# Kernel tuning notes

Hardware: AMD Instinct MI355X
Metric: run time of the kernel (lower is better)

## Reference

```python
import jax, jax.numpy as jnp
import numpy as np

EMBED = 1024
HEADS = 16
HEAD_DIM = EMBED // HEADS


def setup_inputs() -> dict:
    key = jax.random.key(0)
    ks = jax.random.split(key, 5)
    s = 0.02
    x = jax.random.normal(ks[0], (2, 2048, EMBED), dtype=jnp.float32)
    W_qkv = jax.random.normal(ks[1], (EMBED, 3 * EMBED), dtype=jnp.float32) * s
    b_qkv = jnp.zeros((3 * EMBED,), dtype=jnp.float32)
    W_proj = jax.random.normal(ks[2], (EMBED, EMBED), dtype=jnp.float32) * s
    b_proj = jnp.zeros((EMBED,), dtype=jnp.float32)
    return {"x": x, "W_qkv": W_qkv, "b_qkv": b_qkv, "W_proj": W_proj, "b_proj": b_proj}


def reference(x, W_qkv, b_qkv, W_proj, b_proj):
    B, N, _ = x.shape
    scale = HEAD_DIM ** -0.5
    qkv = x @ W_qkv + b_qkv                     # [B,N,3E]
    qkv = qkv.reshape(B, N, 3, HEADS, HEAD_DIM)
    q = qkv[:, :, 0].transpose(0, 2, 1, 3) * scale  # [B,H,N,D]
    k = qkv[:, :, 1].transpose(0, 2, 1, 3)
    v = qkv[:, :, 2].transpose(0, 2, 1, 3)
    attn = jnp.einsum('bhnd,bhmd->bhnm', q, k)  # [B,H,N,N]
    attn = jax.nn.softmax(attn, axis=-1)
    out = jnp.einsum('bhnm,bhmd->bhnd', attn, v)  # [B,H,N,D]
    out = out.transpose(0, 2, 1, 3).reshape(B, N, HEADS * HEAD_DIM)
    return out @ W_proj + b_proj
```

## Files before the change

### kernel.cpp

```cpp
#include <hip/hip_runtime.h>
#include <hip/hip_bf16.h>
#include <stdint.h>

typedef unsigned short u16;
typedef __bf16 bf16x8 __attribute__((ext_vector_type(8)));
typedef float f32x4 __attribute__((ext_vector_type(4)));

__device__ __forceinline__ u16 f2bf(float f) {
    union { float f; unsigned u; } x; x.f = f;
    unsigned u = x.u;
    u += 0x7FFFu + ((u >> 16) & 1u);
    return (u16)(u >> 16);
}

typedef __attribute__((address_space(1))) void gvoid;
typedef __attribute__((address_space(3))) void lvoid;
__device__ __forceinline__ void gl2lds16(const void* g, void* l) {
    __builtin_amdgcn_global_load_lds((gvoid*)g, (lvoid*)l, 16, 0, 0);
}

__global__ __launch_bounds__(256) void prep_kernel(
    const float* __restrict__ x, u16* __restrict__ xb,
    const float* __restrict__ Wqkv, u16* __restrict__ wqkvT,
    const float* __restrict__ Wproj, u16* __restrict__ wprojT)
{
    __shared__ u16 tile[64][65];
    const int blk = blockIdx.x;
    const int tid = threadIdx.x;

    if (blk < 2048) {
        const size_t i = ((size_t)blk * 256 + tid) * 8;
        float4 a = *(const float4*)(x + i);
        float4 b = *(const float4*)(x + i + 4);
        ushort4 oa, ob;
        oa.x = f2bf(a.x); oa.y = f2bf(a.y); oa.z = f2bf(a.z); oa.w = f2bf(a.w);
        ob.x = f2bf(b.x); ob.y = f2bf(b.y); ob.z = f2bf(b.z); ob.w = f2bf(b.w);
        *(ushort4*)(xb + i) = oa;
        *(ushort4*)(xb + i + 4) = ob;
        return;
    }
    const float* in; u16* out; int rows, cols, bx, by;
    if (blk < 2816) { int t = blk - 2048; in = Wqkv;  out = wqkvT;  rows = 1024; cols = 3072; bx = t % 48; by = t / 48; }
    else            { int t = blk - 2816; in = Wproj; out = wprojT; rows = 1024; cols = 1024; bx = t % 16; by = t / 16; }
#pragma unroll
    for (int i = 0; i < 16; i++) {
        int e = i * 256 + tid;
        int r = e >> 6, c = e & 63;
        tile[r][c] = f2bf(in[(size_t)(by * 64 + r) * cols + bx * 64 + c]);
    }
    __syncthreads();
#pragma unroll
    for (int i = 0; i < 16; i++) {
        int e = i * 256 + tid;
        int r = e >> 6, c = e & 63;
        out[(size_t)(bx * 64 + r) * rows + by * 64 + c] = tile[c][r];
    }
}

__global__ __launch_bounds__(256) void transpose_v(
    const u16* __restrict__ in, u16* __restrict__ out)
{
    __shared__ u16 tile[64][65];
    const int bh = blockIdx.y;
    const int t0 = blockIdx.x * 64;
    const u16* ip = in + ((size_t)bh * 2048 + t0) * 64;
    u16* op = out + (size_t)bh * 64 * 2048 + t0;
    const int tid = threadIdx.x;
#pragma unroll
    for (int i = 0; i < 16; i++) {
        int e = i * 256 + tid;
        int r = e >> 6, c = e & 63;
        tile[r][c] = ip[(size_t)r * 64 + c];
    }
    __syncthreads();
#pragma unroll
    for (int i = 0; i < 16; i++) {
        int e = i * 256 + tid;
        int d = e >> 6, tt = e & 63;
        op[(size_t)d * 2048 + tt] = tile[tt][d];
    }
}

__global__ __launch_bounds__(256) void gemm_qkv(
    const u16* __restrict__ A, const u16* __restrict__ Bt,
    const float* __restrict__ bias,
    u16* __restrict__ q, u16* __restrict__ ko, u16* __restrict__ vo)
{
    constexpr int K = 1024;
    __shared__ __align__(16) u16 smem[128 * 132];
    u16* sA = smem;
    u16* sB = smem + 8192;
    const int tid = threadIdx.x;
    const int wave = tid >> 6, lane = tid & 63;
    const int quad = lane >> 4, l16 = lane & 15;
    const int wm = (wave >> 1) * 64, wn = (wave & 1) * 64;
    const int m0 = blockIdx.y * 128, n0 = blockIdx.x * 128;
    const int srow = lane >> 3;
    const int scol = (lane & 7) * 8;

    f32x4 acc[4][4];
#pragma unroll
    for (int i = 0; i < 4; i++)
#pragma unroll
        for (int j = 0; j < 4; j++)
#pragma unroll
            for (int r = 0; r < 4; r++) acc[i][j][r] = 0.f;

    for (int kt = 0; kt < K; kt += 64) {
        __syncthreads();
#pragma unroll
        for (int t = 0; t < 4; t++) {
            int rb = wave * 32 + t * 8;
            gl2lds16(A  + (size_t)(m0 + rb + srow) * K + kt + scol, &sA[rb * 64]);
            gl2lds16(Bt + (size_t)(n0 + rb + srow) * K + kt + scol, &sB[rb * 64]);
        }
        __syncthreads();
#pragma unroll
        for (int kk = 0; kk < 64; kk += 32) {
            bf16x8 af[4], bfr[4];
#pragma unroll
            for (int t = 0; t < 4; t++) {
                af[t]  = *(const bf16x8*)&sA[(wm + t * 16 + l16) * 64 + kk + quad * 8];
                bfr[t] = *(const bf16x8*)&sB[(wn + t * 16 + l16) * 64 + kk + quad * 8];
            }
#pragma unroll
            for (int i = 0; i < 4; i++)
#pragma unroll
                for (int j = 0; j < 4; j++)
                    acc[i][j] = __builtin_amdgcn_mfma_f32_16x16x32_bf16(
                        af[i], bfr[j], acc[i][j], 0, 0, 0);
        }
    }

    const float QSCALE = 0.18033688011112042f;
    __syncthreads();
#pragma unroll
    for (int i = 0; i < 4; i++) {
#pragma unroll
        for (int j = 0; j < 4; j++) {
            int n = n0 + wn + j * 16 + l16;
            float bv = bias[n];
            float sc = (n < 1024) ? QSCALE : 1.0f;
#pragma unroll
            for (int r = 0; r < 4; r++) {
                float v = (acc[i][j][r] + bv) * sc;
                smem[(wm + i * 16 + quad * 4 + r) * 132 + wn + j * 16 + l16] = f2bf(v);
            }
        }
    }
    __syncthreads();

#pragma unroll
    for (int it = 0; it < 8; it++) {
        int c = it * 256 + tid;
        int m_l = c >> 4;
        int n8 = (c & 15) * 8;
        uint4 w = *(const uint4*)&smem[m_l * 132 + n8];
        int n = n0 + n8;
        int which = n >> 10, rem = n & 1023;
        int h = rem >> 6, d = rem & 63;
        int m = m0 + m_l;
        int b = m >> 11, t = m & 2047;
        u16* dst = (which == 0) ? q : (which == 1) ? ko : vo;
        *(uint4*)(dst + ((size_t)(b * 16 + h) * 2048 + t) * 64 + d) = w;
    }
}

__global__ __launch_bounds__(256) void attn_kernel(
    const u16* __restrict__ q, const u16* __restrict__ ko,
    const u16* __restrict__ vt, u16* __restrict__ o)
{
    __shared__ __align__(16) u16 sQ[128 * 72];
    __shared__ __align__(16) u16 sK[64 * 72];
    __shared__ __align__(16) u16 sV[64 * 72];
    __shared__ __align__(16) u16 sP[128 * 72];

    const int tid = threadIdx.x;
    const int wave = tid >> 6, lane = tid & 63;
    const int quad = lane >> 4, l16 = lane & 15;

    const int lid = blockIdx.x;
    const int xcd = lid & 7, idx = lid >> 3;
    const int h = xcd * 2 + (idx & 1);
    const int b = (idx >> 1) & 1;
    const int q0 = (idx >> 2) * 128;
    const size_t bh = (size_t)(b * 16 + h);

    const u16* qp  = q  + bh * 2048 * 64;
    const u16* kp  = ko + bh * 2048 * 64;
    const u16* vtp = vt + bh * 64 * 2048;

    const int sr0 = tid >> 3;
    const int sc0 = (tid & 7) * 8;
    const int sr1 = (tid + 256) >> 3;

#pragma unroll
    for (int i = 0; i < 4; i++) {
        int c = tid + i * 256;
        int r = c >> 3, cc = c & 7;
        *(uint4*)&sQ[r * 72 + cc * 8] =
            *(const uint4*)(qp + (size_t)(q0 + r) * 64 + cc * 8);
    }

    union { uint32_t u[4]; bf16x8 v; } ones;
    ones.u[0] = ones.u[1] = ones.u[2] = ones.u[3] = 0x3F803F80u;

    uint4 pk0 = *(const uint4*)(kp + (size_t)sr0 * 64 + sc0);
    uint4 pk1 = *(const uint4*)(kp + (size_t)sr1 * 64 + sc0);
    uint4 pv0 = *(const uint4*)(vtp + (size_t)sr0 * 2048 + sc0);
    uint4 pv1 = *(const uint4*)(vtp + (size_t)sr1 * 2048 + sc0);

    __syncthreads();

    bf16x8 qf[2][2];
#pragma unroll
    for (int i = 0; i < 2; i++)
#pragma unroll
        for (int k2 = 0; k2 < 2; k2++)
            qf[i][k2] = *(const bf16x8*)&sQ[(wave * 32 + i * 16 + l16) * 72 + k2 * 32 + quad * 8];

    f32x4 accO[2][4];
    f32x4 accL[2];
#pragma unroll
    for (int i = 0; i < 2; i++) {
#pragma unroll
        for (int r = 0; r < 4; r++) accL[i][r] = 0.f;
#pragma unroll
        for (int j = 0; j < 4; j++)
#pragma unroll
            for (int r = 0; r < 4; r++) accO[i][j][r] = 0.f;
    }

    for (int kt = 0; kt < 2048; kt += 64) {
        __syncthreads();
        *(uint4*)&sK[sr0 * 72 + sc0] = pk0;
        *(uint4*)&sK[sr1 * 72 + sc0] = pk1;
        *(uint4*)&sV[sr0 * 72 + sc0] = pv0;
        *(uint4*)&sV[sr1 * 72 + sc0] = pv1;
        if (kt + 64 < 2048) {
            int nt = kt + 64;
            pk0 = *(const uint4*)(kp + (size_t)(nt + sr0) * 64 + sc0);
            pk1 = *(const uint4*)(kp + (size_t)(nt + sr1) * 64 + sc0);
            pv0 = *(const uint4*)(vtp + (size_t)sr0 * 2048 + nt + sc0);
            pv1 = *(const uint4*)(vtp + (size_t)sr1 * 2048 + nt + sc0);
        }
        __syncthreads();

        f32x4 S[2][4];
#pragma unroll
        for (int i = 0; i < 2; i++)
#pragma unroll
            for (int j = 0; j < 4; j++)
#pragma unroll
                for (int r = 0; r < 4; r++) S[i][j][r] = 0.f;
#pragma unroll
        for (int k2 = 0; k2 < 2; k2++) {
            int kk = k2 * 32;
#pragma unroll
            for (int j = 0; j < 4; j++) {
                bf16x8 bk = *(const bf16x8*)&sK[(j * 16 + l16) * 72 + kk + quad * 8];
                S[0][j] = __builtin_amdgcn_mfma_f32_16x16x32_bf16(qf[0][k2], bk, S[0][j], 0, 0, 0);
                S[1][j] = __builtin_amdgcn_mfma_f32_16x16x32_bf16(qf[1][k2], bk, S[1][j], 0, 0, 0);
            }
        }

        u16* pw = &sP[(wave * 32 + quad * 4) * 72 + l16];
#pragma unroll
        for (int i = 0; i < 2; i++)
#pragma unroll
            for (int j = 0; j < 4; j++)
#pragma unroll
                for (int r = 0; r < 4; r++) {
                    union { float f; uint32_t u; } e;
                    e.f = __builtin_amdgcn_exp2f(S[i][j][r]);
                    pw[(i * 16 + r) * 72 + j * 16] = (u16)(e.u >> 16);
                }

#pragma unroll
        for (int k2 = 0; k2 < 2; k2++) {
            int kk = k2 * 32;
            bf16x8 bv[4];
#pragma unroll
            for (int j = 0; j < 4; j++)
                bv[j] = *(const bf16x8*)&sV[(j * 16 + l16) * 72 + kk + quad * 8];
#pragma unroll
            for (int i = 0; i < 2; i++) {
                bf16x8 ap = *(const bf16x8*)&sP[(wave * 32 + i * 16 + l16) * 72 + kk + quad * 8];
#pragma unroll
                for (int j = 0; j < 4; j++)
                    accO[i][j] = __builtin_amdgcn_mfma_f32_16x16x32_bf16(ap, bv[j], accO[i][j], 0, 0, 0);
                accL[i] = __builtin_amdgcn_mfma_f32_16x16x32_bf16(ap, ones.v, accL[i], 0, 0, 0);
            }
        }
    }

#pragma unroll
    for (int i = 0; i < 2; i++)
#pragma unroll
        for (int r = 0; r < 4; r++) {
            float inv = 1.f / accL[i][r];
            size_t row = (size_t)b * 2048 + q0 + wave * 32 + i * 16 + quad * 4 + r;
#pragma unroll
            for (int j = 0; j < 4; j++)
                o[row * 1024 + h * 64 + j * 16 + l16] = f2bf(accO[i][j][r] * inv);
        }
}

__global__ __launch_bounds__(256) void gemm_proj(
    const u16* __restrict__ A, const u16* __restrict__ Bt,
    const float* __restrict__ bias, float* __restrict__ out)
{
    constexpr int K = 1024;
    __shared__ __align__(16) u16 sA[128 * 64];
    __shared__ __align__(16) u16 sB[128 * 64];
    const int tid = threadIdx.x;
    const int wave = tid >> 6, lane = tid & 63;
    const int quad = lane >> 4, l16 = lane & 15;
    const int wm = (wave >> 1) * 64, wn = (wave & 1) * 64;
    const int m0 = blockIdx.y * 128, n0 = blockIdx.x * 128;
    const int srow = lane >> 3;
    const int scol = (lane & 7) * 8;

    f32x4 acc[4][4];
#pragma unroll
    for (int i = 0; i < 4; i++)
#pragma unroll
        for (int j = 0; j < 4; j++)
#pragma unroll
            for (int r = 0; r < 4; r++) acc[i][j][r] = 0.f;

    for (int kt = 0; kt < K; kt += 64) {
        __syncthreads();
#pragma unroll
        for (int t = 0; t < 4; t++) {
            int rb = wave * 32 + t * 8;
            gl2lds16(A  + (size_t)(m0 + rb + srow) * K + kt + scol, &sA[rb * 64]);
            gl2lds16(Bt + (size_t)(n0 + rb + srow) * K + kt + scol, &sB[rb * 64]);
        }
        __syncthreads();
#pragma unroll
        for (int kk = 0; kk < 64; kk += 32) {
            bf16x8 af[4], bfr[4];
#pragma unroll
            for (int t = 0; t < 4; t++) {
                af[t]  = *(const bf16x8*)&sA[(wm + t * 16 + l16) * 64 + kk + quad * 8];
                bfr[t] = *(const bf16x8*)&sB[(wn + t * 16 + l16) * 64 + kk + quad * 8];
            }
#pragma unroll
            for (int i = 0; i < 4; i++)
#pragma unroll
                for (int j = 0; j < 4; j++)
                    acc[i][j] = __builtin_amdgcn_mfma_f32_16x16x32_bf16(
                        af[i], bfr[j], acc[i][j], 0, 0, 0);
        }
    }

#pragma unroll
    for (int i = 0; i < 4; i++) {
#pragma unroll
        for (int j = 0; j < 4; j++) {
            int n = n0 + wn + j * 16 + l16;
            float bv = bias[n];
#pragma unroll
            for (int r = 0; r < 4; r++) {
                int m = m0 + wm + i * 16 + quad * 4 + r;
                out[(size_t)m * 1024 + n] = acc[i][j][r] + bv;
            }
        }
    }
}

extern "C" void kernel_launch(void* const* d_in, const int* in_sizes, int n_in,
                              void* d_out, int out_size, void* d_ws, size_t ws_size,
                              hipStream_t stream) {
    const float* x     = (const float*)d_in[0];
    const float* Wqkv  = (const float*)d_in[1];
    const float* bqkv  = (const float*)d_in[2];
    const float* Wproj = (const float*)d_in[3];
    const float* bproj = (const float*)d_in[4];
    float* out = (float*)d_out;
    char* ws = (char*)d_ws;

    u16* wqkvT  = (u16*)(ws);
    u16* wprojT = (u16*)(ws +  6291456);
    u16* xb     = (u16*)(ws +  8388608);
    u16* qb     = (u16*)(ws + 16777216);
    u16* kb     = (u16*)(ws + 25165824);
    u16* vtb    = (u16*)(ws + 33554432);
    u16* ob     = (u16*)(ws + 41943040);
    u16* vb     = ob;

    prep_kernel<<<dim3(3072), 256, 0, stream>>>(x, xb, Wqkv, wqkvT, Wproj, wprojT);
    gemm_qkv<<<dim3(24, 32), 256, 0, stream>>>(xb, wqkvT, bqkv, qb, kb, vb);
    transpose_v<<<dim3(32, 32), 256, 0, stream>>>(vb, vtb);
    attn_kernel<<<dim3(512), 256, 0, stream>>>(qb, kb, vtb, ob);
    gemm_proj<<<dim3(8, 32), 256, 0, stream>>>(ob, wprojT, bproj, out);
}
```

Baseline: 218.5 us.

## Fuse V transpose into QKV GEMM epilogue and halve attention query tile

```diff
diff --git a/kernel.cpp b/kernel.cpp
--- a/kernel.cpp
+++ b/kernel.cpp
@@ -57,34 +57,10 @@
     }
 }
 
-__global__ __launch_bounds__(256) void transpose_v(
-    const u16* __restrict__ in, u16* __restrict__ out)
-{
-    __shared__ u16 tile[64][65];
-    const int bh = blockIdx.y;
-    const int t0 = blockIdx.x * 64;
-    const u16* ip = in + ((size_t)bh * 2048 + t0) * 64;
-    u16* op = out + (size_t)bh * 64 * 2048 + t0;
-    const int tid = threadIdx.x;
-#pragma unroll
-    for (int i = 0; i < 16; i++) {
-        int e = i * 256 + tid;
-        int r = e >> 6, c = e & 63;
-        tile[r][c] = ip[(size_t)r * 64 + c];
-    }
-    __syncthreads();
-#pragma unroll
-    for (int i = 0; i < 16; i++) {
-        int e = i * 256 + tid;
-        int d = e >> 6, tt = e & 63;
-        op[(size_t)d * 2048 + tt] = tile[tt][d];
-    }
-}
-
 __global__ __launch_bounds__(256) void gemm_qkv(
     const u16* __restrict__ A, const u16* __restrict__ Bt,
     const float* __restrict__ bias,
-    u16* __restrict__ q, u16* __restrict__ ko, u16* __restrict__ vo)
+    u16* __restrict__ q, u16* __restrict__ ko, u16* __restrict__ vt)
 {
     constexpr int K = 1024;
     __shared__ __align__(16) u16 smem[128 * 132];
@@ -133,14 +109,13 @@
     }
 
     const float QSCALE = 0.18033688011112042f;
+    const float sc = (n0 < 1024) ? QSCALE : 1.0f;
     __syncthreads();
 #pragma unroll
     for (int i = 0; i < 4; i++) {
 #pragma unroll
         for (int j = 0; j < 4; j++) {
-            int n = n0 + wn + j * 16 + l16;
-            float bv = bias[n];
-            float sc = (n < 1024) ? QSCALE : 1.0f;
+            float bv = bias[n0 + wn + j * 16 + l16];
 #pragma unroll
             for (int r = 0; r < 4; r++) {
                 float v = (acc[i][j][r] + bv) * sc;
@@ -150,19 +125,36 @@
     }
     __syncthreads();
 
-#pragma unroll
-    for (int it = 0; it < 8; it++) {
-        int c = it * 256 + tid;
-        int m_l = c >> 4;
-        int n8 = (c & 15) * 8;
-        uint4 w = *(const uint4*)&smem[m_l * 132 + n8];
-        int n = n0 + n8;
-        int which = n >> 10, rem = n & 1023;
-        int h = rem >> 6, d = rem & 63;
-        int m = m0 + m_l;
-        int b = m >> 11, t = m & 2047;
-        u16* dst = (which == 0) ? q : (which == 1) ? ko : vo;
-        *(uint4*)(dst + ((size_t)(b * 16 + h) * 2048 + t) * 64 + d) = w;
+    if (n0 < 2048) {
+        u16* dst = (n0 < 1024) ? q : ko;
+#pragma unroll
+        for (int it = 0; it < 8; it++) {
+            int c = it * 256 + tid;
+            int m_l = c >> 4;
+            int n8 = (c & 15) * 8;
+            uint4 w = *(const uint4*)&smem[m_l * 132 + n8];
+            int n = n0 + n8;
+            int h = (n & 1023) >> 6, d = n & 63;
+            int m = m0 + m_l;
+            int b = m >> 11, t = m & 2047;
+            *(uint4*)(dst + ((size_t)(b * 16 + h) * 2048 + t) * 64 + d) = w;
+        }
+    } else {
+        int nv = n0 - 2048;
+        int n_l = tid & 127, mh = tid >> 7;
+        int hh = (nv >> 6) + (n_l >> 6);
+        int d = n_l & 63;
+        int bb = m0 >> 11, t0 = m0 & 2047;
+        u16* vrow = vt + ((size_t)(bb * 16 + hh) * 64 + d) * 2048 + t0 + mh * 64;
+#pragma unroll
+        for (int it = 0; it < 8; it++) {
+            int tch = mh * 64 + it * 8;
+            union { u16 s[8]; uint4 w; } pk;
+#pragma unroll
+            for (int i = 0; i < 8; i++)
+                pk.s[i] = smem[(tch + i) * 132 + n_l];
+            *(uint4*)(vrow + it * 8) = pk.w;
+        }
     }
 }
 
@@ -170,10 +162,9 @@
     const u16* __restrict__ q, const u16* __restrict__ ko,
     const u16* __restrict__ vt, u16* __restrict__ o)
 {
-    __shared__ __align__(16) u16 sQ[128 * 72];
+    __shared__ __align__(16) u16 sQP[64 * 72];
     __shared__ __align__(16) u16 sK[64 * 72];
     __shared__ __align__(16) u16 sV[64 * 72];
-    __shared__ __align__(16) u16 sP[128 * 72];
 
     const int tid = threadIdx.x;
     const int wave = tid >> 6, lane = tid & 63;
@@ -183,7 +174,7 @@
     const int xcd = lid & 7, idx = lid >> 3;
     const int h = xcd * 2 + (idx & 1);
     const int b = (idx >> 1) & 1;
-    const int q0 = (idx >> 2) * 128;
+    const int q0 = (idx >> 2) * 64;
     const size_t bh = (size_t)(b * 16 + h);
 
     const u16* qp  = q  + bh * 2048 * 64;
@@ -192,13 +183,13 @@
 
     const int sr0 = tid >> 3;
     const int sc0 = (tid & 7) * 8;
-    const int sr1 = (tid + 256) >> 3;
-
-#pragma unroll
-    for (int i = 0; i < 4; i++) {
+    const int sr1 = sr0 + 32;
+
+#pragma unroll
+    for (int i = 0; i < 2; i++) {
         int c = tid + i * 256;
         int r = c >> 3, cc = c & 7;
-        *(uint4*)&sQ[r * 72 + cc * 8] =
+        *(uint4*)&sQP[r * 72 + cc * 8] =
             *(const uint4*)(qp + (size_t)(q0 + r) * 64 + cc * 8);
     }
 
@@ -212,24 +203,20 @@
 
     __syncthreads();
 
-    bf16x8 qf[2][2];
-#pragma unroll
-    for (int i = 0; i < 2; i++)
-#pragma unroll
-        for (int k2 = 0; k2 < 2; k2++)
-            qf[i][k2] = *(const bf16x8*)&sQ[(wave * 32 + i * 16 + l16) * 72 + k2 * 32 + quad * 8];
-
-    f32x4 accO[2][4];
-    f32x4 accL[2];
-#pragma unroll
-    for (int i = 0; i < 2; i++) {
-#pragma unroll
-        for (int r = 0; r < 4; r++) accL[i][r] = 0.f;
-#pragma unroll
-        for (int j = 0; j < 4; j++)
-#pragma unroll
-            for (int r = 0; r < 4; r++) accO[i][j][r] = 0.f;
-    }
+    bf16x8 qf[2];
+#pragma unroll
+    for (int k2 = 0; k2 < 2; k2++)
+        qf[k2] = *(const bf16x8*)&sQP[(wave * 16 + l16) * 72 + k2 * 32 + quad * 8];
+    __syncthreads();
+
+    f32x4 accO[4];
+    f32x4 accL;
+#pragma unroll
+    for (int r = 0; r < 4; r++) accL[r] = 0.f;
+#pragma unroll
+    for (int j = 0; j < 4; j++)
+#pragma unroll
+        for (int r = 0; r < 4; r++) accO[j][r] = 0.f;
 
     for (int kt = 0; kt < 2048; kt += 64) {
         __syncthreads();
@@ -246,64 +233,52 @@
         }
         __syncthreads();
 
-        f32x4 S[2][4];
-#pragma unroll
-        for (int i = 0; i < 2; i++)
-#pragma unroll
-            for (int j = 0; j < 4; j++)
-#pragma unroll
-                for (int r = 0; r < 4; r++) S[i][j][r] = 0.f;
+        f32x4 S[4];
+#pragma unroll
+        for (int j = 0; j < 4; j++)
+#pragma unroll
+            for (int r = 0; r < 4; r++) S[j][r] = 0.f;
 #pragma unroll
         for (int k2 = 0; k2 < 2; k2++) {
             int kk = k2 * 32;
 #pragma unroll
             for (int j = 0; j < 4; j++) {
                 bf16x8 bk = *(const bf16x8*)&sK[(j * 16 + l16) * 72 + kk + quad * 8];
-                S[0][j] = __builtin_amdgcn_mfma_f32_16x16x32_bf16(qf[0][k2], bk, S[0][j], 0, 0, 0);
-                S[1][j] = __builtin_amdgcn_mfma_f32_16x16x32_bf16(qf[1][k2], bk, S[1][j], 0, 0, 0);
-            }
-        }
-
-        u16* pw = &sP[(wave * 32 + quad * 4) * 72 + l16];
-#pragma unroll
-        for (int i = 0; i < 2; i++)
-#pragma unroll
-            for (int j = 0; j < 4; j++)
-#pragma unroll
-                for (int r = 0; r < 4; r++) {
-                    union { float f; uint32_t u; } e;
-                    e.f = __builtin_amdgcn_exp2f(S[i][j][r]);
-                    pw[(i * 16 + r) * 72 + j * 16] = (u16)(e.u >> 16);
-                }
+                S[j] = __builtin_amdgcn_mfma_f32_16x16x32_bf16(qf[k2], bk, S[j], 0, 0, 0);
+            }
+        }
+
+        u16* pw = &sQP[(wave * 16 + quad * 4) * 72 + l16];
+#pragma unroll
+        for (int j = 0; j < 4; j++)
+#pragma unroll
+            for (int r = 0; r < 4; r++) {
+                union { float f; uint32_t u; } e;
+                e.f = __builtin_amdgcn_exp2f(S[j][r]);
+                pw[r * 72 + j * 16] = (u16)(e.u >> 16);
+            }
 
 #pragma unroll
         for (int k2 = 0; k2 < 2; k2++) {
             int kk = k2 * 32;
-            bf16x8 bv[4];
-#pragma unroll
-            for (int j = 0; j < 4; j++)
-                bv[j] = *(const bf16x8*)&sV[(j * 16 + l16) * 72 + kk + quad * 8];
-#pragma unroll
-            for (int i = 0; i < 2; i++) {
-                bf16x8 ap = *(const bf16x8*)&sP[(wave * 32 + i * 16 + l16) * 72 + kk + quad * 8];
-#pragma unroll
-                for (int j = 0; j < 4; j++)
-                    accO[i][j] = __builtin_amdgcn_mfma_f32_16x16x32_bf16(ap, bv[j], accO[i][j], 0, 0, 0);
-                accL[i] = __builtin_amdgcn_mfma_f32_16x16x32_bf16(ap, ones.v, accL[i], 0, 0, 0);
-            }
-        }
-    }
-
-#pragma unroll
-    for (int i = 0; i < 2; i++)
-#pragma unroll
-        for (int r = 0; r < 4; r++) {
-            float inv = 1.f / accL[i][r];
-            size_t row = (size_t)b * 2048 + q0 + wave * 32 + i * 16 + quad * 4 + r;
-#pragma unroll
-            for (int j = 0; j < 4; j++)
-                o[row * 1024 + h * 64 + j * 16 + l16] = f2bf(accO[i][j][r] * inv);
-        }
+            bf16x8 ap = *(const bf16x8*)&sQP[(wave * 16 + l16) * 72 + kk + quad * 8];
+#pragma unroll
+            for (int j = 0; j < 4; j++) {
+                bf16x8 bv = *(const bf16x8*)&sV[(j * 16 + l16) * 72 + kk + quad * 8];
+                accO[j] = __builtin_amdgcn_mfma_f32_16x16x32_bf16(ap, bv, accO[j], 0, 0, 0);
+            }
+            accL = __builtin_amdgcn_mfma_f32_16x16x32_bf16(ap, ones.v, accL, 0, 0, 0);
+        }
+    }
+
+#pragma unroll
+    for (int r = 0; r < 4; r++) {
+        float inv = 1.f / accL[r];
+        size_t row = (size_t)b * 2048 + q0 + wave * 16 + quad * 4 + r;
+#pragma unroll
+        for (int j = 0; j < 4; j++)
+            o[row * 1024 + h * 64 + j * 16 + l16] = f2bf(accO[j][r] * inv);
+    }
 }
 
 __global__ __launch_bounds__(256) void gemm_proj(
@@ -388,11 +363,9 @@
     u16* kb     = (u16*)(ws + 25165824);
     u16* vtb    = (u16*)(ws + 33554432);
     u16* ob     = (u16*)(ws + 41943040);
-    u16* vb     = ob;
 
     prep_kernel<<<dim3(3072), 256, 0, stream>>>(x, xb, Wqkv, wqkvT, Wproj, wprojT);
-    gemm_qkv<<<dim3(24, 32), 256, 0, stream>>>(xb, wqkvT, bqkv, qb, kb, vb);
-    transpose_v<<<dim3(32, 32), 256, 0, stream>>>(vb, vtb);
-    attn_kernel<<<dim3(512), 256, 0, stream>>>(qb, kb, vtb, ob);
+    gemm_qkv<<<dim3(24, 32), 256, 0, stream>>>(xb, wqkvT, bqkv, qb, kb, vtb);
+    attn_kernel<<<dim3(1024), 256, 0, stream>>>(qb, kb, vtb, ob);
     gemm_proj<<<dim3(8, 32), 256, 0, stream>>>(ob, wprojT, bproj, out);
 }
```

After: 224.7 us. +2.9%, slower.
